# Optimization experiments

Hardware: AMD Instinct MI355X
Metric: run time of the kernel (lower is better)

Reference implementation:

```python
import jax, jax.numpy as jnp
import numpy as np

N_ATOMS = 100000
N_BONDS = 200000
N_MOLS = 4000
ATOMS_PER_MOL = 25
MAX_NB = 6
ATOM_FDIM = 133
BOND_FDIM = 14
HIDDEN = 300
DEPTH = 3


def setup_inputs() -> dict:
    key = jax.random.key(0)
    ks = jax.random.split(key, 8)
    f_atoms = jax.random.normal(ks[0], (N_ATOMS, ATOM_FDIM), dtype=jnp.float32)
    f_bonds = jax.random.normal(ks[1], (N_BONDS, BOND_FDIM), dtype=jnp.float32)
    # incoming-bond lists per atom (irregular gather targets)
    a2b = jax.random.randint(ks[2], (N_ATOMS, MAX_NB), 0, N_BONDS, dtype=jnp.int32)
    # source atom of each directed bond
    b2a = jax.random.randint(ks[3], (N_BONDS,), 0, N_ATOMS, dtype=jnp.int32)
    # reverse bond: directed bonds come in pairs (2i, 2i+1)
    b2revb = (jnp.arange(N_BONDS, dtype=jnp.int32) ^ 1)
    # contiguous [start, size] per molecule
    starts = jnp.arange(N_MOLS, dtype=jnp.int32) * ATOMS_PER_MOL
    sizes = jnp.full((N_MOLS,), ATOMS_PER_MOL, dtype=jnp.int32)
    a_scope = jnp.stack([starts, sizes], axis=1)
    W_i = jax.random.normal(ks[4], (HIDDEN, ATOM_FDIM + BOND_FDIM), dtype=jnp.float32) * 0.05
    W_h = jax.random.normal(ks[5], (HIDDEN, HIDDEN), dtype=jnp.float32) * 0.05
    W_o = jax.random.normal(ks[6], (HIDDEN, ATOM_FDIM + HIDDEN), dtype=jnp.float32) * 0.05
    b_o = jax.random.normal(ks[7], (HIDDEN,), dtype=jnp.float32) * 0.05
    return {"f_atoms": f_atoms, "f_bonds": f_bonds, "a2b": a2b, "b2a": b2a,
            "b2revb": b2revb, "a_scope": a_scope, "W_i": W_i, "W_h": W_h,
            "W_o": W_o, "b_o": b_o}


def reference(f_atoms, f_bonds, a2b, b2a, b2revb, a_scope, W_i, W_h, W_o, b_o):
    # initial directed-bond messages: [f_atoms[src], f_bonds] -> Linear -> ReLU
    input_feats = jnp.concatenate([f_atoms[b2a], f_bonds], axis=1)  # (E, 147)
    message = jax.nn.relu(input_feats @ W_i.T)  # (E, H)
    for _ in range(DEPTH - 1):
        nei_a_message = message[a2b].sum(axis=1)          # (V, H) gather+sum
        nei_message = nei_a_message[b2a] - message[b2revb]  # (E, H)
        message = jax.nn.relu(nei_message @ W_h.T)
    a_message = message[a2b].sum(axis=1)  # (V, H)
    atom_hiddens = jax.nn.relu(jnp.concatenate([f_atoms, a_message], axis=1) @ W_o.T + b_o)
    # vectorized scope mean-pool (scopes are contiguous ranges)
    starts = a_scope[:, 0]
    sizes = a_scope[:, 1]
    seg_ids = jnp.searchsorted(starts, jnp.arange(atom_hiddens.shape[0]), side='right') - 1
    sums = jax.ops.segment_sum(atom_hiddens, seg_ids, num_segments=N_MOLS)
    denom = jnp.maximum(sizes, 1).astype(atom_hiddens.dtype)[:, None]
    mol_vecs = jnp.where((sizes > 0)[:, None], sums / denom, 0.0)
    return mol_vecs
```

## Files before the change

### kernel.cpp

```cpp
#include <hip/hip_runtime.h>
#include <stdint.h>

#define N_ATOMS   100000
#define N_BONDS   200000
#define N_MOLS    4000
#define MAX_NB    6
#define ATOM_FDIM 133
#define BOND_FDIM 14
#define HIDDEN    300
#define NPAD      320

typedef __attribute__((ext_vector_type(8))) short          bf16x8;
typedef __attribute__((ext_vector_type(8))) unsigned short u16x8;
typedef __attribute__((ext_vector_type(4))) float          f32x4;
typedef __attribute__((ext_vector_type(4))) unsigned int   u32x4;

static __device__ __forceinline__ float u2f(unsigned int u) {
  union { unsigned int u; float f; } v; v.u = u; return v.f;
}
static __device__ __forceinline__ unsigned int f2u(float f) {
  union { float f; unsigned int u; } v; v.f = f; return v.u;
}
static __device__ __forceinline__ float bflo(unsigned int u) { return u2f(u << 16); }
static __device__ __forceinline__ float bfhi(unsigned int u) { return u2f(u & 0xffff0000u); }
static __device__ __forceinline__ unsigned short f2bf_rn(float f) {
  unsigned int u = f2u(f);
  return (unsigned short)((u + 0x7fffu + ((u >> 16) & 1u)) >> 16);
}
static __device__ __forceinline__ unsigned int pack_rn(float lo, float hi) {
  return ((unsigned int)f2bf_rn(hi) << 16) | f2bf_rn(lo);
}

__global__ __launch_bounds__(256) void convin_kernel(
    const float* __restrict__ w, unsigned short* __restrict__ o, int N, int K, int KP) {
  size_t total = (size_t)N * KP;
  for (size_t idx = (size_t)blockIdx.x * 256 + threadIdx.x; idx < total; idx += (size_t)gridDim.x * 256) {
    int n = (int)(idx / KP), k = (int)(idx - (size_t)n * KP);
    float v = (k < K) ? w[(size_t)n * K + k] : 0.f;
    o[idx] = f2bf_rn(v);
  }
}

__global__ __launch_bounds__(256) void convw_kernel(
    const float* __restrict__ w, unsigned short* __restrict__ o,
    int Ksrc, int seg1, int src2off, int seg2dst, int seg2len, int KP) {
  int total = NPAD * KP;
  for (int idx = blockIdx.x * 256 + threadIdx.x; idx < total; idx += gridDim.x * 256) {
    int n = idx / KP, k = idx - n * KP;
    int src = -1;
    if (k < seg1) src = k;
    else if (k >= seg2dst && k < seg2dst + seg2len) src = src2off + (k - seg2dst);
    float v = (n < HIDDEN && src >= 0) ? w[(size_t)n * Ksrc + src] : 0.f;
    o[idx] = f2bf_rn(v);
  }
}

template<int KP, int SEG, bool RELU>
__global__ __launch_bounds__(256) void gemm_tp(
    const unsigned short* S1, const unsigned short* __restrict__ S2,
    const int* __restrict__ gmap, const unsigned short* __restrict__ W,
    unsigned short* out, int M, int nTiles) {
  constexpr int CHUNKS = KP / 8;
  constexpr int NST    = KP / 32;
  __shared__ __align__(16) unsigned short As[2 * 64 * KP];

  const int tid  = threadIdx.x;
  const int lane = tid & 63;
  const int wv   = tid >> 6;
  const int ar   = lane & 15, kq = lane >> 4;
  const int nbase = wv * 80;
  const unsigned short* Wl = W + (size_t)(nbase + ar) * KP + kq * 8;

  auto rowof = [&](int tile) { int r = tile * 64 + lane; return (r < M) ? r : (M - 1); };

  auto stage = [&](int buf, int drow, int srow) {
    char* base = (char*)As + (size_t)buf * (64 * KP * 2);
#pragma unroll
    for (int cs = wv; cs < CHUNKS; cs += 4) {
      const unsigned short* src;
      if (SEG == 0) src = S1 + (size_t)drow * KP + cs * 8;
      else src = (cs < 20) ? (S1 + (size_t)srow * 160 + cs * 8)
                           : (S2 + (size_t)drow * 32 + (cs - 20) * 8);
      __builtin_amdgcn_global_load_lds(
          (const __attribute__((address_space(1))) void*)src,
          (__attribute__((address_space(3))) void*)(base + (size_t)cs * 1024), 16, 0, 0);
    }
  };

  f32x4 acc[4][5];

  auto compute = [&](int buf) {
    const char* base = (const char*)As + (size_t)buf * (64 * KP * 2);
    bf16x8 bnxt[5];
#pragma unroll
    for (int nf = 0; nf < 5; nf++) bnxt[nf] = *(const bf16x8*)(Wl + (size_t)nf * 16 * KP);
#pragma unroll
    for (int ks = 0; ks < NST; ks++) {
      bf16x8 bcur[5];
#pragma unroll
      for (int nf = 0; nf < 5; nf++) bcur[nf] = bnxt[nf];
      if (ks + 1 < NST) {
#pragma unroll
        for (int nf = 0; nf < 5; nf++)
          bnxt[nf] = *(const bf16x8*)(Wl + (size_t)nf * 16 * KP + (ks + 1) * 32);
      }
      bf16x8 af[4];
#pragma unroll
      for (int m = 0; m < 4; m++)
        af[m] = *(const bf16x8*)(base + (size_t)((ks * 4 + kq) * 64 + m * 16 + ar) * 16);
#pragma unroll
      for (int nf = 0; nf < 5; nf++)
#pragma unroll
        for (int m = 0; m < 4; m++)
          acc[m][nf] = __builtin_amdgcn_mfma_f32_16x16x32_bf16(af[m], bcur[nf], acc[m][nf], 0, 0, 0);
    }
  };

  auto storeC = [&](int tile) {
#pragma unroll
    for (int m = 0; m < 4; m++)
#pragma unroll
      for (int rr = 0; rr < 4; rr++) {
        int orow = tile * 64 + m * 16 + kq * 4 + rr;
        if (orow >= M) continue;
#pragma unroll
        for (int nf = 0; nf < 5; nf++) {
          float v = acc[m][nf][rr];
          if (RELU) v = v > 0.f ? v : 0.f;
          out[(size_t)orow * NPAD + nbase + nf * 16 + ar] = f2bf_rn(v);
        }
      }
  };

  int t = blockIdx.x;
  if (t >= nTiles) return;
  {
    int srow0 = (SEG == 1) ? gmap[rowof(t)] : 0;
    stage(0, rowof(t), srow0);
  }
  int tn = t + gridDim.x;
  int g_n = (SEG == 1 && tn < nTiles) ? gmap[rowof(tn)] : 0;
  __syncthreads();

  int cur = 0;
  while (t < nTiles) {
    const int nxt = t + gridDim.x;
    if (nxt < nTiles) stage(cur ^ 1, rowof(nxt), g_n);
    const int t2 = nxt + gridDim.x;
    int g_n2 = (SEG == 1 && t2 < nTiles) ? gmap[rowof(t2)] : 0;
#pragma unroll
    for (int m = 0; m < 4; m++)
#pragma unroll
      for (int n = 0; n < 5; n++) acc[m][n] = (f32x4){0.f, 0.f, 0.f, 0.f};
    compute(cur);
    __syncthreads();
    storeC(t);
    cur ^= 1; t = nxt; g_n = g_n2;
  }
}

template<int KP, int SRC, bool RELU, bool BIAS>
__global__ __launch_bounds__(256, 2) void gemm_bp(
    const float* __restrict__ Af, const float* __restrict__ F2,
    const unsigned short* Ab, const unsigned short* __restrict__ Nei,
    const int* __restrict__ gmap, const unsigned short* __restrict__ W,
    const float* __restrict__ bias, unsigned short* out, int M) {
  constexpr int NST = KP / 32;
  __shared__ __align__(16) unsigned short As[NST * 2048];

  const int b0   = blockIdx.x * 64;
  const int tid  = threadIdx.x;
  const int lane = tid & 63;
  const int wave = tid >> 6;
  const int sr   = tid >> 2;
  const int q    = tid & 3;

  int row = b0 + sr;
  if (row >= M) row = M - 1;
  const int dbase = (sr >> 4) * 512 + (q * 16 + (sr & 15)) * 8;

  auto stage_chunk = [&](int ks) -> u16x8 {
    const int kc = ks * 32 + q * 8;
    u16x8 r;
    if (kc >= 160) {
      r = *(const u16x8*)(Ab + (size_t)row * NPAD + (kc - 160));
    } else {
#pragma unroll
      for (int j = 0; j < 8; j++) {
        int k = kc + j;
        r[j] = (k < ATOM_FDIM) ? f2bf_rn(Af[(size_t)row * ATOM_FDIM + k]) : (unsigned short)0;
      }
    }
    return r;
  };

  constexpr int G = 5;
#pragma unroll
  for (int ks0 = 0; ks0 < NST; ks0 += G) {
    u16x8 vals[G];
#pragma unroll
    for (int j = 0; j < G; j++) { int ks = ks0 + j; if (ks < NST) vals[j] = stage_chunk(ks); }
#pragma unroll
    for (int j = 0; j < G; j++) { int ks = ks0 + j; if (ks < NST) *(u16x8*)&As[ks * 2048 + dbase] = vals[j]; }
  }
  __syncthreads();

  f32x4 acc[4][5];
#pragma unroll
  for (int m = 0; m < 4; m++)
#pragma unroll
    for (int n = 0; n < 5; n++) acc[m][n] = (f32x4){0.f, 0.f, 0.f, 0.f};

  const int nbase = wave * 80;
  const int ar = lane & 15, kq = lane >> 4;
  const unsigned short* Wl = W + (size_t)(nbase + ar) * KP + kq * 8;

  bf16x8 bnxt[5];
#pragma unroll
  for (int nf = 0; nf < 5; nf++) bnxt[nf] = *(const bf16x8*)(Wl + (size_t)nf * 16 * KP);

#pragma unroll
  for (int ks = 0; ks < NST; ks++) {
    bf16x8 bcur[5];
#pragma unroll
    for (int nf = 0; nf < 5; nf++) bcur[nf] = bnxt[nf];
    if (ks + 1 < NST) {
#pragma unroll
      for (int nf = 0; nf < 5; nf++)
        bnxt[nf] = *(const bf16x8*)(Wl + (size_t)nf * 16 * KP + (ks + 1) * 32);
    }
    bf16x8 af[4];
#pragma unroll
    for (int m = 0; m < 4; m++) af[m] = *(const bf16x8*)&As[ks * 2048 + m * 512 + lane * 8];
#pragma unroll
    for (int nf = 0; nf < 5; nf++)
#pragma unroll
      for (int m = 0; m < 4; m++)
        acc[m][nf] = __builtin_amdgcn_mfma_f32_16x16x32_bf16(af[m], bcur[nf], acc[m][nf], 0, 0, 0);
  }

#pragma unroll
  for (int m = 0; m < 4; m++) {
#pragma unroll
    for (int rr = 0; rr < 4; rr++) {
      int orow = b0 + m * 16 + kq * 4 + rr;
      if (orow >= M) continue;
#pragma unroll
      for (int nf = 0; nf < 5; nf++) {
        int ocol = nbase + nf * 16 + ar;
        float v = acc[m][nf][rr];
        if (BIAS) v += (ocol < HIDDEN) ? bias[ocol] : 0.f;
        if (RELU) v = v > 0.f ? v : 0.f;
        out[(size_t)orow * NPAD + ocol] = f2bf_rn(v);
      }
    }
  }
}

__global__ __launch_bounds__(256) void agg_kernel(
    const unsigned short* __restrict__ src, const int* __restrict__ a2b,
    unsigned short* __restrict__ dst) {
  const int TPA = NPAD / 16;
  int idx = blockIdx.x * 256 + threadIdx.x;
  if (idx >= N_ATOMS * TPA) return;
  int a  = idx / TPA;
  int kc = (idx - a * TPA) * 16;
  int bidx[MAX_NB];
#pragma unroll
  for (int j = 0; j < MAX_NB; j++) bidx[j] = a2b[a * MAX_NB + j];
  float slo[8], shi[8];
#pragma unroll
  for (int t = 0; t < 8; t++) { slo[t] = 0.f; shi[t] = 0.f; }
#pragma unroll
  for (int j = 0; j < MAX_NB; j++) {
    const u32x4* p = (const u32x4*)(src + (size_t)bidx[j] * NPAD + kc);
    u32x4 v0 = p[0], v1 = p[1];
#pragma unroll
    for (int t = 0; t < 4; t++) {
      slo[t]     += bflo(v0[t]); shi[t]     += bfhi(v0[t]);
      slo[4 + t] += bflo(v1[t]); shi[4 + t] += bfhi(v1[t]);
    }
  }
  u32x4 o0, o1;
#pragma unroll
  for (int t = 0; t < 4; t++) { o0[t] = pack_rn(slo[t], shi[t]); o1[t] = pack_rn(slo[4 + t], shi[4 + t]); }
  u32x4* qp = (u32x4*)(dst + (size_t)a * NPAD + kc);
  qp[0] = o0; qp[1] = o1;
}

__global__ __launch_bounds__(256) void combineH_kernel(
    const unsigned short* __restrict__ neiZ, const unsigned short* Zh,
    const int* __restrict__ b2a, unsigned short* msg) {
  const int TPB = NPAD / 16;
  const int NPAIR = N_BONDS / 2;
  int idx = blockIdx.x * 256 + threadIdx.x;
  if (idx >= NPAIR * TPB) return;
  int p  = idx / TPB;
  int kc = (idx - p * TPB) * 16;
  int b0i = 2 * p, b1i = 2 * p + 1;
  int g0 = b2a[b0i], g1 = b2a[b1i];
  const u32x4* pn0 = (const u32x4*)(neiZ + (size_t)g0 * NPAD + kc);
  const u32x4* pn1 = (const u32x4*)(neiZ + (size_t)g1 * NPAD + kc);
  const u32x4* pz0 = (const u32x4*)(Zh + (size_t)b1i * NPAD + kc);
  const u32x4* pz1 = (const u32x4*)(Zh + (size_t)b0i * NPAD + kc);
  u32x4 n00 = pn0[0], n01 = pn0[1], n10 = pn1[0], n11 = pn1[1];
  u32x4 z00 = pz0[0], z01 = pz0[1], z10 = pz1[0], z11 = pz1[1];
  u32x4 o00, o01, o10, o11;
#pragma unroll
  for (int t = 0; t < 4; t++) {
    float a, c;
    a = bflo(n00[t]) - bflo(z00[t]); c = bfhi(n00[t]) - bfhi(z00[t]);
    o00[t] = pack_rn(a > 0.f ? a : 0.f, c > 0.f ? c : 0.f);
    a = bflo(n01[t]) - bflo(z01[t]); c = bfhi(n01[t]) - bfhi(z01[t]);
    o01[t] = pack_rn(a > 0.f ? a : 0.f, c > 0.f ? c : 0.f);
    a = bflo(n10[t]) - bflo(z10[t]); c = bfhi(n10[t]) - bfhi(z10[t]);
    o10[t] = pack_rn(a > 0.f ? a : 0.f, c > 0.f ? c : 0.f);
    a = bflo(n11[t]) - bflo(z11[t]); c = bfhi(n11[t]) - bfhi(z11[t]);
    o11[t] = pack_rn(a > 0.f ? a : 0.f, c > 0.f ? c : 0.f);
  }
  u32x4* q0 = (u32x4*)(msg + (size_t)b0i * NPAD + kc);
  u32x4* q1 = (u32x4*)(msg + (size_t)b1i * NPAD + kc);
  q0[0] = o00; q0[1] = o01; q1[0] = o10; q1[1] = o11;
}

__global__ __launch_bounds__(256) void readout_kernel(
    const unsigned short* __restrict__ hidden, const int* __restrict__ a_scope,
    float* __restrict__ out) {
  const int TPM = NPAD / 8;
  int idx = blockIdx.x * 256 + threadIdx.x;
  if (idx >= N_MOLS * TPM) return;
  int m = idx / TPM;
  int c = (idx - m * TPM) * 8;
  int start = a_scope[m * 2], size = a_scope[m * 2 + 1];
  float s[8];
#pragma unroll
  for (int t = 0; t < 8; t++) s[t] = 0.f;
  for (int i = 0; i < size; i++) {
    const u32x4 v = *(const u32x4*)(hidden + (size_t)(start + i) * NPAD + c);
#pragma unroll
    for (int t = 0; t < 4; t++) { s[2 * t] += bflo(v[t]); s[2 * t + 1] += bfhi(v[t]); }
  }
  float inv = (size > 0) ? 1.f / (float)size : 0.f;
#pragma unroll
  for (int t = 0; t < 8; t++) {
    int col = c + t;
    if (col < HIDDEN) out[(size_t)m * HIDDEN + col] = s[t] * inv;
  }
}

extern "C" void kernel_launch(void* const* d_in, const int* in_sizes, int n_in,
                              void* d_out, int out_size, void* d_ws, size_t ws_size,
                              hipStream_t stream) {
  const float* f_atoms = (const float*)d_in[0];
  const float* f_bonds = (const float*)d_in[1];
  const int*   a2b     = (const int*)d_in[2];
  const int*   b2a     = (const int*)d_in[3];
  const int*   a_scope = (const int*)d_in[5];
  const float* W_i     = (const float*)d_in[6];
  const float* W_h     = (const float*)d_in[7];
  const float* W_o     = (const float*)d_in[8];
  const float* b_o     = (const float*)d_in[9];
  float* out = (float*)d_out;

  char* ws = (char*)d_ws;
  size_t off = 0;
  auto alloc = [&](size_t bytes) { size_t o = off; off += (bytes + 255) & ~(size_t)255; return o; };
  unsigned short* P     = (unsigned short*)(ws + alloc((size_t)N_BONDS * NPAD * 2));
  unsigned short* R     = (unsigned short*)(ws + alloc((size_t)N_ATOMS * NPAD * 2));
  unsigned short* fa_bf = (unsigned short*)(ws + alloc((size_t)N_ATOMS * 160 * 2));
  unsigned short* fb_bf = (unsigned short*)(ws + alloc((size_t)N_BONDS * 32 * 2));
  unsigned short* WiAB  = (unsigned short*)(ws + alloc((size_t)NPAD * 192 * 2));
  unsigned short* Wh    = (unsigned short*)(ws + alloc((size_t)NPAD * 320 * 2));
  unsigned short* Wo    = (unsigned short*)(ws + alloc((size_t)NPAD * 480 * 2));

  convin_kernel<<<2048, 256, 0, stream>>>(f_atoms, fa_bf, N_ATOMS, ATOM_FDIM, 160);
  convin_kernel<<<2048, 256, 0, stream>>>(f_bonds, fb_bf, N_BONDS, BOND_FDIM, 32);
  convw_kernel<<<(NPAD * 192 + 255) / 256, 256, 0, stream>>>(W_i, WiAB, 147, 133, 133, 160, 14, 192);
  convw_kernel<<<(NPAD * 320 + 255) / 256, 256, 0, stream>>>(W_h, Wh, 300, 300, 0, 0, 0, 320);
  convw_kernel<<<(NPAD * 480 + 255) / 256, 256, 0, stream>>>(W_o, Wo, 433, 133, 133, 160, 300, 480);

  const int nTilesB = N_BONDS / 64;
  const int gagg = (N_ATOMS * (NPAD / 16) + 255) / 256;
  const int gpar = ((N_BONDS / 2) * (NPAD / 16) + 255) / 256;
  const int gridA = (N_ATOMS + 63) / 64;

  gemm_tp<192, 1, true><<<768, 256, 0, stream>>>(
      fa_bf, fb_bf, b2a, WiAB, P, N_BONDS, nTilesB);

  gemm_tp<320, 0, false><<<512, 256, 0, stream>>>(
      P, nullptr, nullptr, Wh, P, N_BONDS, nTilesB);
  agg_kernel<<<gagg, 256, 0, stream>>>(P, a2b, R);
  combineH_kernel<<<gpar, 256, 0, stream>>>(R, P, b2a, P);

  gemm_tp<320, 0, false><<<512, 256, 0, stream>>>(
      P, nullptr, nullptr, Wh, P, N_BONDS, nTilesB);
  agg_kernel<<<gagg, 256, 0, stream>>>(P, a2b, R);
  combineH_kernel<<<gpar, 256, 0, stream>>>(R, P, b2a, P);

  agg_kernel<<<gagg, 256, 0, stream>>>(P, a2b, R);
  gemm_bp<480, 2, true, true><<<gridA, 256, 0, stream>>>(
      f_atoms, nullptr, R, nullptr, nullptr, Wo, b_o, R, N_ATOMS);
  readout_kernel<<<(N_MOLS * (NPAD / 8) + 255) / 256, 256, 0, stream>>>(R, a_scope, out);
}
```

Measured before the change: 668.8 us.

## Fuse combine step into W_h GEMM staging and reuse persistent GEMM for output layer

The second message-passing step now uses a new persistent GEMM kernel. As it stages each tile, it gathers the aggregated atom rows and the reverse-bond messages, subtracts them, applies ReLU and writes the result into LDS as bf16. This removes one separate combineH pass and its full read-write of the bond message buffer. The output-layer GEMM moves from the one-shot gemm_bp kernel, which converted f_atoms from fp32 per element, to the persistent double-buffered gemm_tp, which reads the pre-converted bf16 atom features and adds the bias. The price is register-staged gathers inside the GEMM, which may raise register pressure and lower occupancy; the kernels also run in place on P, which relies on the row-tile ordering.

```diff
diff --git a/kernel.cpp b/kernel.cpp
--- a/kernel.cpp
+++ b/kernel.cpp
@@ -55,11 +55,11 @@
   }
 }
 
-template<int KP, int SEG, bool RELU>
+template<int KP, int SEG, bool RELU, bool BIAS>
 __global__ __launch_bounds__(256) void gemm_tp(
-    const unsigned short* S1, const unsigned short* __restrict__ S2,
+    const unsigned short* S1, const unsigned short* S2,
     const int* __restrict__ gmap, const unsigned short* __restrict__ W,
-    unsigned short* out, int M, int nTiles) {
+    const float* __restrict__ bias, unsigned short* out, int M, int nTiles) {
   constexpr int CHUNKS = KP / 8;
   constexpr int NST    = KP / 32;
   __shared__ __align__(16) unsigned short As[2 * 64 * KP];
@@ -78,9 +78,11 @@
 #pragma unroll
     for (int cs = wv; cs < CHUNKS; cs += 4) {
       const unsigned short* src;
-      if (SEG == 0) src = S1 + (size_t)drow * KP + cs * 8;
-      else src = (cs < 20) ? (S1 + (size_t)srow * 160 + cs * 8)
-                           : (S2 + (size_t)drow * 32 + (cs - 20) * 8);
+      if (SEG == 0)      src = S1 + (size_t)drow * KP + cs * 8;
+      else if (SEG == 1) src = (cs < 20) ? (S1 + (size_t)srow * 160 + cs * 8)
+                                         : (S2 + (size_t)drow * 32 + (cs - 20) * 8);
+      else               src = (cs < 20) ? (S1 + (size_t)drow * 160 + cs * 8)
+                                         : (S2 + (size_t)drow * NPAD + (cs - 20) * 8);
       __builtin_amdgcn_global_load_lds(
           (const __attribute__((address_space(1))) void*)src,
           (__attribute__((address_space(3))) void*)(base + (size_t)cs * 1024), 16, 0, 0);
@@ -125,9 +127,11 @@
         if (orow >= M) continue;
 #pragma unroll
         for (int nf = 0; nf < 5; nf++) {
+          int ocol = nbase + nf * 16 + ar;
           float v = acc[m][nf][rr];
+          if (BIAS) v += (ocol < HIDDEN) ? bias[ocol] : 0.f;
           if (RELU) v = v > 0.f ? v : 0.f;
-          out[(size_t)orow * NPAD + nbase + nf * 16 + ar] = f2bf_rn(v);
+          out[(size_t)orow * NPAD + ocol] = f2bf_rn(v);
         }
       }
   };
@@ -159,101 +163,112 @@
   }
 }
 
-template<int KP, int SRC, bool RELU, bool BIAS>
-__global__ __launch_bounds__(256, 2) void gemm_bp(
-    const float* __restrict__ Af, const float* __restrict__ F2,
-    const unsigned short* Ab, const unsigned short* __restrict__ Nei,
-    const int* __restrict__ gmap, const unsigned short* __restrict__ W,
-    const float* __restrict__ bias, unsigned short* out, int M) {
-  constexpr int NST = KP / 32;
-  __shared__ __align__(16) unsigned short As[NST * 2048];
-
-  const int b0   = blockIdx.x * 64;
+__global__ __launch_bounds__(256) void gemm_tpf(
+    const unsigned short* Z, const unsigned short* __restrict__ Nei,
+    const int* __restrict__ b2a, const unsigned short* __restrict__ W,
+    unsigned short* out, int nTiles) {
+  constexpr int KP = 320, NST = 10, NREG = 10;
+  __shared__ __align__(16) unsigned short As[2 * 64 * KP];
+
   const int tid  = threadIdx.x;
   const int lane = tid & 63;
-  const int wave = tid >> 6;
-  const int sr   = tid >> 2;
-  const int q    = tid & 3;
-
-  int row = b0 + sr;
-  if (row >= M) row = M - 1;
-  const int dbase = (sr >> 4) * 512 + (q * 16 + (sr & 15)) * 8;
-
-  auto stage_chunk = [&](int ks) -> u16x8 {
-    const int kc = ks * 32 + q * 8;
-    u16x8 r;
-    if (kc >= 160) {
-      r = *(const u16x8*)(Ab + (size_t)row * NPAD + (kc - 160));
-    } else {
-#pragma unroll
-      for (int j = 0; j < 8; j++) {
-        int k = kc + j;
-        r[j] = (k < ATOM_FDIM) ? f2bf_rn(Af[(size_t)row * ATOM_FDIM + k]) : (unsigned short)0;
+  const int wv   = tid >> 6;
+  const int ar   = lane & 15, kq = lane >> 4;
+  const int nbase = wv * 80;
+  const unsigned short* Wl = W + (size_t)(nbase + ar) * KP + kq * 8;
+
+  u32x4 nei4[NREG], z4[NREG];
+
+  auto loadreg = [&](int tile) {
+    const int row = tile * 64 + lane;
+    const int g   = b2a[row];
+    const int rev = row ^ 1;
+#pragma unroll
+    for (int i = 0; i < NREG; i++) {
+      const int cs = i * 4 + wv;
+      nei4[i] = *(const u32x4*)(Nei + (size_t)g * NPAD + cs * 8);
+      z4[i]   = *(const u32x4*)(Z + (size_t)rev * NPAD + cs * 8);
+    }
+  };
+
+  auto writestage = [&](int buf) {
+    char* base = (char*)As + (size_t)buf * (64 * KP * 2);
+#pragma unroll
+    for (int i = 0; i < NREG; i++) {
+      const int cs = i * 4 + wv;
+      u32x4 o;
+#pragma unroll
+      for (int t4 = 0; t4 < 4; t4++) {
+        float lo = bflo(nei4[i][t4]) - bflo(z4[i][t4]);
+        float hi = bfhi(nei4[i][t4]) - bfhi(z4[i][t4]);
+        lo = lo > 0.f ? lo : 0.f; hi = hi > 0.f ? hi : 0.f;
+        o[t4] = pack_rn(lo, hi);
       }
-    }
-    return r;
-  };
-
-  constexpr int G = 5;
-#pragma unroll
-  for (int ks0 = 0; ks0 < NST; ks0 += G) {
-    u16x8 vals[G];
-#pragma unroll
-    for (int j = 0; j < G; j++) { int ks = ks0 + j; if (ks < NST) vals[j] = stage_chunk(ks); }
-#pragma unroll
-    for (int j = 0; j < G; j++) { int ks = ks0 + j; if (ks < NST) *(u16x8*)&As[ks * 2048 + dbase] = vals[j]; }
-  }
+      *(u32x4*)(base + (size_t)(cs * 64 + lane) * 16) = o;
+    }
+  };
+
+  f32x4 acc[4][5];
+
+  auto compute = [&](int buf) {
+    const char* base = (const char*)As + (size_t)buf * (64 * KP * 2);
+    bf16x8 bnxt[5];
+#pragma unroll
+    for (int nf = 0; nf < 5; nf++) bnxt[nf] = *(const bf16x8*)(Wl + (size_t)nf * 16 * KP);
+#pragma unroll
+    for (int ks = 0; ks < NST; ks++) {
+      bf16x8 bcur[5];
+#pragma unroll
+      for (int nf = 0; nf < 5; nf++) bcur[nf] = bnxt[nf];
+      if (ks + 1 < NST) {
+#pragma unroll
+        for (int nf = 0; nf < 5; nf++)
+          bnxt[nf] = *(const bf16x8*)(Wl + (size_t)nf * 16 * KP + (ks + 1) * 32);
+      }
+      bf16x8 af[4];
+#pragma unroll
+      for (int m = 0; m < 4; m++)
+        af[m] = *(const bf16x8*)(base + (size_t)((ks * 4 + kq) * 64 + m * 16 + ar) * 16);
+#pragma unroll
+      for (int nf = 0; nf < 5; nf++)
+#pragma unroll
+        for (int m = 0; m < 4; m++)
+          acc[m][nf] = __builtin_amdgcn_mfma_f32_16x16x32_bf16(af[m], bcur[nf], acc[m][nf], 0, 0, 0);
+    }
+  };
+
+  auto storeC = [&](int tile) {
+#pragma unroll
+    for (int m = 0; m < 4; m++)
+#pragma unroll
+      for (int rr = 0; rr < 4; rr++) {
+        int orow = tile * 64 + m * 16 + kq * 4 + rr;
+#pragma unroll
+        for (int nf = 0; nf < 5; nf++)
+          out[(size_t)orow * NPAD + nbase + nf * 16 + ar] =
+              f2bf_rn(acc[m][nf][rr]);
+      }
+  };
+
+  int t = blockIdx.x;
+  if (t >= nTiles) return;
+  loadreg(t);
+  writestage(0);
   __syncthreads();
 
-  f32x4 acc[4][5];
-#pragma unroll
-  for (int m = 0; m < 4; m++)
-#pragma unroll
-    for (int n = 0; n < 5; n++) acc[m][n] = (f32x4){0.f, 0.f, 0.f, 0.f};
-
-  const int nbase = wave * 80;
-  const int ar = lane & 15, kq = lane >> 4;
-  const unsigned short* Wl = W + (size_t)(nbase + ar) * KP + kq * 8;
-
-  bf16x8 bnxt[5];
-#pragma unroll
-  for (int nf = 0; nf < 5; nf++) bnxt[nf] = *(const bf16x8*)(Wl + (size_t)nf * 16 * KP);
-
-#pragma unroll
-  for (int ks = 0; ks < NST; ks++) {
-    bf16x8 bcur[5];
-#pragma unroll
-    for (int nf = 0; nf < 5; nf++) bcur[nf] = bnxt[nf];
-    if (ks + 1 < NST) {
-#pragma unroll
-      for (int nf = 0; nf < 5; nf++)
-        bnxt[nf] = *(const bf16x8*)(Wl + (size_t)nf * 16 * KP + (ks + 1) * 32);
-    }
-    bf16x8 af[4];
-#pragma unroll
-    for (int m = 0; m < 4; m++) af[m] = *(const bf16x8*)&As[ks * 2048 + m * 512 + lane * 8];
-#pragma unroll
-    for (int nf = 0; nf < 5; nf++)
-#pragma unroll
-      for (int m = 0; m < 4; m++)
-        acc[m][nf] = __builtin_amdgcn_mfma_f32_16x16x32_bf16(af[m], bcur[nf], acc[m][nf], 0, 0, 0);
-  }
-
-#pragma unroll
-  for (int m = 0; m < 4; m++) {
-#pragma unroll
-    for (int rr = 0; rr < 4; rr++) {
-      int orow = b0 + m * 16 + kq * 4 + rr;
-      if (orow >= M) continue;
-#pragma unroll
-      for (int nf = 0; nf < 5; nf++) {
-        int ocol = nbase + nf * 16 + ar;
-        float v = acc[m][nf][rr];
-        if (BIAS) v += (ocol < HIDDEN) ? bias[ocol] : 0.f;
-        if (RELU) v = v > 0.f ? v : 0.f;
-        out[(size_t)orow * NPAD + ocol] = f2bf_rn(v);
-      }
-    }
+  int cur = 0;
+  while (t < nTiles) {
+    const int nxt = t + gridDim.x;
+    if (nxt < nTiles) loadreg(nxt);
+#pragma unroll
+    for (int m = 0; m < 4; m++)
+#pragma unroll
+      for (int n = 0; n < 5; n++) acc[m][n] = (f32x4){0.f, 0.f, 0.f, 0.f};
+    compute(cur);
+    if (nxt < nTiles) writestage(cur ^ 1);
+    __syncthreads();
+    storeC(t);
+    cur ^= 1; t = nxt;
   }
 }
 
@@ -380,25 +395,25 @@
   convw_kernel<<<(NPAD * 480 + 255) / 256, 256, 0, stream>>>(W_o, Wo, 433, 133, 133, 160, 300, 480);
 
   const int nTilesB = N_BONDS / 64;
+  const int nTilesA = (N_ATOMS + 63) / 64;
   const int gagg = (N_ATOMS * (NPAD / 16) + 255) / 256;
   const int gpar = ((N_BONDS / 2) * (NPAD / 16) + 255) / 256;
-  const int gridA = (N_ATOMS + 63) / 64;
-
-  gemm_tp<192, 1, true><<<768, 256, 0, stream>>>(
-      fa_bf, fb_bf, b2a, WiAB, P, N_BONDS, nTilesB);
-
-  gemm_tp<320, 0, false><<<512, 256, 0, stream>>>(
-      P, nullptr, nullptr, Wh, P, N_BONDS, nTilesB);
+
+  gemm_tp<192, 1, true, false><<<768, 256, 0, stream>>>(
+      fa_bf, fb_bf, b2a, WiAB, nullptr, P, N_BONDS, nTilesB);
+
+  gemm_tp<320, 0, false, false><<<512, 256, 0, stream>>>(
+      P, nullptr, nullptr, Wh, nullptr, P, N_BONDS, nTilesB);
+  agg_kernel<<<gagg, 256, 0, stream>>>(P, a2b, R);
+
+  gemm_tpf<<<512, 256, 0, stream>>>(P, R, b2a, Wh, P, nTilesB);
+
   agg_kernel<<<gagg, 256, 0, stream>>>(P, a2b, R);
   combineH_kernel<<<gpar, 256, 0, stream>>>(R, P, b2a, P);
 
-  gemm_tp<320, 0, false><<<512, 256, 0, stream>>>(
-      P, nullptr, nullptr, Wh, P, N_BONDS, nTilesB);
   agg_kernel<<<gagg, 256, 0, stream>>>(P, a2b, R);
-  combineH_kernel<<<gpar, 256, 0, stream>>>(R, P, b2a, P);
-
-  agg_kernel<<<gagg, 256, 0, stream>>>(P, a2b, R);
-  gemm_bp<480, 2, true, true><<<gridA, 256, 0, stream>>>(
-      f_atoms, nullptr, R, nullptr, nullptr, Wo, b_o, R, N_ATOMS);
+  gemm_tp<480, 3, true, true><<<256, 256, 0, stream>>>(
+      fa_bf, R, nullptr, Wo, b_o, R, N_ATOMS, nTilesA);
+
   readout_kernel<<<(N_MOLS * (NPAD / 8) + 255) / 256, 256, 0, stream>>>(R, a_scope, out);
 }
```

After: 658.8 us. No clear change (-1.5%).
